# Performance work log

Hardware: AMD Instinct MI355X
Metric: run time of the kernel (lower is better)

## Reference

```python
import jax, jax.numpy as jnp
import numpy as np

DIM = 256
CDIM = 512
HEADS = 8
DIM_HEAD = 32
HID = HEADS * DIM_HEAD          # 256
MLP_DIM = int(DIM * 2.5)        # 640
B, T, TC = 8, 8192, 8192
GROUPS = 32
EPS = 1e-5


def setup_inputs() -> dict:
    key = jax.random.key(0)
    ks = jax.random.split(key, 12)
    w = lambda k, shape: jax.random.normal(k, shape, jnp.float32) * 0.02
    return {
        "x": jax.random.normal(ks[0], (B, DIM, T), jnp.float32),
        "c": jax.random.normal(ks[1], (B, CDIM, TC), jnp.float32),
        # self-attn (LinearAttention)
        "W_qkv": w(ks[2], (3 * HID, DIM)),
        "W_so": w(ks[3], (DIM, HID)), "b_so": jnp.zeros((DIM,), jnp.float32),
        "sa_g": jnp.ones((DIM,), jnp.float32), "sa_b": jnp.zeros((DIM,), jnp.float32),
        # cross-attn (LinearAttentionC)
        "W_cq": w(ks[4], (HID, DIM)),
        "W_ckv": w(ks[5], (2 * HID, CDIM)),
        "W_co": w(ks[6], (DIM, HID)), "b_co": jnp.zeros((DIM,), jnp.float32),
        "ca_g": jnp.ones((DIM,), jnp.float32), "ca_b": jnp.zeros((DIM,), jnp.float32),
        # MLP
        "W_m1": w(ks[7], (MLP_DIM, DIM)), "b_m1": jnp.zeros((MLP_DIM,), jnp.float32),
        "W_m2": w(ks[8], (DIM, MLP_DIM)), "b_m2": jnp.zeros((DIM,), jnp.float32),
        # pre-norms
        "nm_g": jnp.ones((DIM,), jnp.float32), "nm_b": jnp.zeros((DIM,), jnp.float32),
        "nm1_g": jnp.ones((DIM,), jnp.float32), "nm1_b": jnp.zeros((DIM,), jnp.float32),
        "nm2_g": jnp.ones((DIM,), jnp.float32), "nm2_b": jnp.zeros((DIM,), jnp.float32),
        "nm3_g": jnp.ones((CDIM,), jnp.float32), "nm3_b": jnp.zeros((CDIM,), jnp.float32),
    }


def group_norm(x, g, b):
    Bx, C, Tx = x.shape
    xg = x.reshape(Bx, GROUPS, C // GROUPS, Tx)
    mu = xg.mean(axis=(2, 3), keepdims=True)
    var = ((xg - mu) ** 2).mean(axis=(2, 3), keepdims=True)
    xn = ((xg - mu) * jax.lax.rsqrt(var + EPS)).reshape(Bx, C, Tx)
    return xn * g[None, :, None] + b[None, :, None]


def conv1(x, W, b=None):
    # 1x1 Conv1d == channel matmul: W [out, in], x [b, in, t]
    y = jnp.einsum('oc,bct->bot', W, x)
    return y if b is None else y + b[None, :, None]


def split_heads(t):
    Bx, HC, Tx = t.shape
    return t.reshape(Bx, HEADS, HC // HEADS, Tx)  # b h c t


def linear_attention(q, k, v):
    # q,k,v: [b, h, d, t]
    scale = DIM_HEAD ** -0.5
    q = jax.nn.softmax(q, axis=-2) * scale   # softmax over feature dim d
    k = jax.nn.softmax(k, axis=-1)           # softmax over time t
    ctx = jnp.einsum('bhdn,bhen->bhde', k, v)   # [b,h,d,e] tiny per-head context
    out = jnp.einsum('bhde,bhdn->bhen', ctx, q)
    Bx, H, E, Tx = out.shape
    return out.reshape(Bx, H * E, Tx)  # b (h c) t


def reference(x, c, W_qkv, W_so, b_so, sa_g, sa_b,
              W_cq, W_ckv, W_co, b_co, ca_g, ca_b,
              W_m1, b_m1, W_m2, b_m2,
              nm_g, nm_b, nm1_g, nm1_b, nm2_g, nm2_b, nm3_g, nm3_b):
    # --- self linear attention + residual ---
    h = group_norm(x, nm_g, nm_b)
    q, k, v = map(split_heads, jnp.split(conv1(h, W_qkv), 3, axis=1))
    o = linear_attention(q, k, v)
    o = group_norm(conv1(o, W_so, b_so), sa_g, sa_b)
    x = o + x
    # --- cross linear attention + residual ---
    h = group_norm(x, nm1_g, nm1_b)
    cn = group_norm(c, nm3_g, nm3_b)
    q = split_heads(conv1(h, W_cq))
    k, v = map(split_heads, jnp.split(conv1(cn, W_ckv), 2, axis=1))
    o = linear_attention(q, k, v)
    o = group_norm(conv1(o, W_co, b_co), ca_g, ca_b)
    x = o + x
    # --- SiLU MLP + residual ---
    h = group_norm(x, nm2_g, nm2_b)
    h = jax.nn.silu(conv1(h, W_m1, b_m1))
    x = conv1(h, W_m2, b_m2) + x
    return x
```

## Files before the change

### kernel.cpp

```cpp
#include <hip/hip_runtime.h>
#include <cmath>

typedef unsigned short u16;
typedef __attribute__((ext_vector_type(8))) __bf16 bf16x8;
typedef __attribute__((ext_vector_type(4))) float f32x4;

#define DEV static __device__ __forceinline__

DEV float b2f(u16 u){ union{unsigned i; float f;} v; v.i=((unsigned)u)<<16; return v.f; }
DEV u16 f2b(float f){ union{float f; unsigned i;} v; v.f=f; unsigned r = v.i + 0x7FFFu + ((v.i>>16)&1u); return (u16)(r>>16); }

#define GLL(g,l) __builtin_amdgcn_global_load_lds((const __attribute__((address_space(1))) void*)(g), (__attribute__((address_space(3))) void*)(l), 16, 0, 0)

__global__ void k_zero(float* p, int n){ int i = blockIdx.x*256+threadIdx.x; if(i<n) p[i]=0.f; }

__global__ void k_cvtall(const float* __restrict__ s0,const float* __restrict__ s1,
                         const float* __restrict__ s2,const float* __restrict__ s3,
                         const float* __restrict__ s4,const float* __restrict__ s5,
                         const float* __restrict__ s6, u16* __restrict__ d){
  int i = blockIdx.x*256 + threadIdx.x;
  if (i >= 983040) return;
  const float* s; int off;
  if      (i < 196608){ s=s0; off=0; }
  else if (i < 262144){ s=s1; off=196608; }
  else if (i < 327680){ s=s2; off=262144; }
  else if (i < 589824){ s=s3; off=327680; }
  else if (i < 655360){ s=s4; off=589824; }
  else if (i < 819200){ s=s5; off=655360; }
  else                { s=s6; off=819200; }
  d[i] = f2b(s[i-off]);
}

__global__ void k_stats_ct(const float* __restrict__ x, const float* __restrict__ c,
                           float* __restrict__ statx, float* __restrict__ statc){
  const bool isc = blockIdx.x >= 256;
  const int blk = isc ? blockIdx.x - 256 : blockIdx.x;
  const int n = isc ? 131072 : 65536;
  const float* src = isc ? c : x;
  float* stat = isc ? statc : statx;
  const long base = (long)blk * n;
  float s=0.f, s2=0.f;
  const float4* xp = (const float4*)(src+base);
  const int n4 = n>>2;
  for (int i=threadIdx.x; i<n4; i+=256){
    float4 v = xp[i];
    s  += v.x+v.y+v.z+v.w;
    s2 += v.x*v.x+v.y*v.y+v.z*v.z+v.w*v.w;
  }
  __shared__ float a[256], a2[256];
  a[threadIdx.x]=s; a2[threadIdx.x]=s2;
  __syncthreads();
  for (int off=128; off>0; off>>=1){
    if (threadIdx.x < off){ a[threadIdx.x]+=a[threadIdx.x+off]; a2[threadIdx.x]+=a2[threadIdx.x+off]; }
    __syncthreads();
  }
  if (threadIdx.x==0){
    const float mu = a[0]/n;
    const float var = a2[0]/n - mu*mu;
    stat[blk*2]   = mu;
    stat[blk*2+1] = rsqrtf(var + 1e-5f);
  }
}

template<bool WF32>
__global__ void k_trans(const float* __restrict__ src, float* __restrict__ dstF,
                        u16* __restrict__ dstB, const float* __restrict__ stat,
                        const float* __restrict__ gw, const float* __restrict__ bw,
                        int C, int chsh){
  const int b = blockIdx.z;
  const int t0 = blockIdx.x*64, c0 = blockIdx.y*64;
  __shared__ float tile[64][65];
  #pragma unroll
  for (int p=0;p<4;p++){
    const int cc = (threadIdx.x>>4) + p*16, tt = (threadIdx.x&15)*4;
    const float4 v = *(const float4*)&src[((long)b*C + c0+cc)*8192 + t0+tt];
    tile[cc][tt+0]=v.x; tile[cc][tt+1]=v.y; tile[cc][tt+2]=v.z; tile[cc][tt+3]=v.w;
  }
  __syncthreads();
  #pragma unroll
  for (int p=0;p<4;p++){
    const int tt = (threadIdx.x>>4) + p*16, c4 = (threadIdx.x&15)*4;
    float raw[4]; u16 nbi[4];
    #pragma unroll
    for (int j=0;j<4;j++){
      raw[j] = tile[c4+j][tt];
      const int c = c0+c4+j, gr = c>>chsh;
      const float mu = stat[(b*32+gr)*2], rs = stat[(b*32+gr)*2+1];
      nbi[j] = f2b((raw[j]-mu)*rs*gw[c]+bw[c]);
    }
    const long db = ((long)b*8192 + t0+tt)*C + c0+c4;
    ushort4 nb; nb.x=nbi[0]; nb.y=nbi[1]; nb.z=nbi[2]; nb.w=nbi[3];
    *(ushort4*)&dstB[db] = nb;
    if (WF32){ float4 rv = {raw[0],raw[1],raw[2],raw[3]}; *(float4*)&dstF[db] = rv; }
  }
}

template<bool OUTB, bool BIAS, bool SILU, bool RES, bool STATS>
__global__ __launch_bounds__(256,2) void k_gemm(
    const u16* __restrict__ A, const u16* __restrict__ W,
    float* __restrict__ outF, u16* __restrict__ outB,
    const float* __restrict__ bias, const float* __restrict__ res,
    float* __restrict__ stat, int K, int O)
{
  __shared__ u16 As[128*64];
  __shared__ u16 Ws[128*64];
  __shared__ float sb[128][2];
  const int tid = threadIdx.x;
  const int wv = tid>>6, lane = tid&63;
  const long t0 = (long)blockIdx.y*128;
  const int o0 = blockIdx.x*128;
  const int wt = (wv>>1)*64, wo = (wv&1)*64;
  const int lr = lane>>3, lc = (lane&7)*8;
  f32x4 acc[4][4] = {};
  for (int kc = 0; kc < K; kc += 64){
    #pragma unroll
    for (int it = 0; it < 4; ++it){
      const int r = wv*32 + it*8;
      GLL(A + (t0 + r + lr)*(long)K + kc + lc, &As[r*64]);
      GLL(W + (long)(o0 + r + lr)*K + kc + lc, &Ws[r*64]);
    }
    __syncthreads();
    #pragma unroll
    for (int ks=0; ks<2; ++ks){
      const int kb = ks*32 + (lane>>4)*8;
      bf16x8 af[4], bfr[4];
      #pragma unroll
      for (int i=0;i<4;i++) af[i]  = *(const bf16x8*)&As[(wt + i*16 + (lane&15))*64 + kb];
      #pragma unroll
      for (int j=0;j<4;j++) bfr[j] = *(const bf16x8*)&Ws[(wo + j*16 + (lane&15))*64 + kb];
      #pragma unroll
      for (int i=0;i<4;i++)
        #pragma unroll
        for (int j=0;j<4;j++)
          acc[i][j] = __builtin_amdgcn_mfma_f32_16x16x32_bf16(af[i], bfr[j], acc[i][j], 0, 0, 0);
    }
    __syncthreads();
  }
  if (STATS){
    if (tid < 128){ sb[tid][0]=0.f; sb[tid][1]=0.f; }
    __syncthreads();
  }
  const int q = lane>>4, cc = lane&15;
  #pragma unroll
  for (int j=0;j<4;j++){
    const int o = o0 + wo + j*16 + cc;
    const float bv = BIAS ? bias[o] : 0.f;
    float ts=0.f, ts2=0.f;
    #pragma unroll
    for (int i=0;i<4;i++){
      const long tb = t0 + wt + i*16 + q*4;
      #pragma unroll
      for (int r=0;r<4;r++){
        float v = acc[i][j][r] + bv;
        if (SILU) v = v * (1.f/(1.f + __expf(-v)));
        const long idx = (tb + r)*(long)O + o;
        if (RES) v += res[idx];
        if (STATS){ ts += v; ts2 += v*v; }
        if (OUTB) outB[idx] = f2b(v); else outF[idx] = v;
      }
    }
    if (STATS){
      const int ol = wo + j*16 + cc;
      atomicAdd(&sb[ol][0], ts);
      atomicAdd(&sb[ol][1], ts2);
    }
  }
  if (STATS){
    __syncthreads();
    if (tid < 16){
      float u=0.f, u2=0.f;
      #pragma unroll
      for (int j2=0;j2<8;j2++){ u += sb[tid*8+j2][0]; u2 += sb[tid*8+j2][1]; }
      const int bb = (int)(t0>>13);
      atomicAdd(&stat[(bb*32 + (o0>>3) + tid)*2],   u);
      atomicAdd(&stat[(bb*32 + (o0>>3) + tid)*2+1], u2);
    }
  }
}

__global__ __launch_bounds__(256,2) void k_ctx(const u16* __restrict__ kvp, float* __restrict__ part,
                      int stride, int koff, int voff){
  const int tid = threadIdx.x;
  const int b = blockIdx.x >> 6, seg = blockIdx.x & 63;
  const int h = tid>>5, d = tid&31;
  __shared__ u16 kb[16][256];
  __shared__ float vf[16][260];
  float acc[32];
  #pragma unroll
  for (int e=0;e<32;e++) acc[e]=0.f;
  float ks = 0.f;
  const long rb = ((long)b*8192 + seg*128)*stride;
  const int w = tid>>6, sub = tid&63;
  for (int tc=0; tc<128; tc+=16){
    #pragma unroll
    for (int p=0;p<4;p++){
      const int row = p*4 + w;
      const long rowbase = rb + (long)(tc+row)*stride;
      if (sub < 32){
        uint4 val = *(const uint4*)(kvp + rowbase + koff + sub*8);
        *(uint4*)&kb[row][sub*8] = val;
      } else {
        const int s2 = sub-32;
        uint4 val = *(const uint4*)(kvp + rowbase + voff + s2*8);
        const u16* vs = (const u16*)&val;
        float4 f0 = {b2f(vs[0]),b2f(vs[1]),b2f(vs[2]),b2f(vs[3])};
        float4 f1 = {b2f(vs[4]),b2f(vs[5]),b2f(vs[6]),b2f(vs[7])};
        *(float4*)&vf[row][s2*8] = f0;
        *(float4*)&vf[row][s2*8+4] = f1;
      }
    }
    __syncthreads();
    #pragma unroll
    for (int r=0;r<16;r++){
      const float kpv = __expf(b2f(kb[r][h*32+d]));
      ks += kpv;
      #pragma unroll
      for (int e4=0;e4<8;e4++){
        const float4 v4 = *(const float4*)&vf[r][h*32+e4*4];
        acc[e4*4+0] += kpv*v4.x; acc[e4*4+1] += kpv*v4.y;
        acc[e4*4+2] += kpv*v4.z; acc[e4*4+3] += kpv*v4.w;
      }
    }
    __syncthreads();
  }
  float* pb = part + (long)blockIdx.x*8448;
  #pragma unroll
  for (int e=0;e<32;e++) pb[e*256 + tid] = acc[e];
  pb[8192 + tid] = ks;
}

__global__ void k_ctxred(const float* __restrict__ part, float* __restrict__ ctx,
                         float* __restrict__ ksumF){
  if (blockIdx.x >= 256){
    const int j = (blockIdx.x-256)*256 + threadIdx.x;
    #pragma unroll
    for (int q=0;q<4;q++){
      const int idx = j*4+q;
      const int b = idx>>8, cch = idx&255;
      float s=0.f;
      for (int g=0; g<64; g++) s += part[((long)(b*64+g))*8448 + 8192 + cch];
      ksumF[idx] = s;
    }
    return;
  }
  const int i = blockIdx.x*256 + threadIdx.x;
  const int b = i>>13, r = i&8191;
  float s=0.f;
  for (int g=0; g<64; g++) s += part[((long)(b*64+g))*8448 + r];
  ctx[i] = s;
}

__global__ void k_attnout(const u16* __restrict__ q, const float* __restrict__ ctx,
                          const float* __restrict__ ksumF,
                          u16* __restrict__ out, int stride, int qoff){
  const int b = blockIdx.x >> 8, t0 = (blockIdx.x & 255)*32;
  __shared__ float cs[8512];
  for (int i=threadIdx.x; i<8192; i+=256){
    const int e=i>>8, cch=i&255;
    cs[(cch>>5)*1064 + (cch&31)*33 + e] = ctx[(b<<13) + i] / ksumF[b*256 + cch];
  }
  __syncthreads();
  const int t = t0 + (threadIdx.x>>3), h = threadIdx.x&7;
  const u16* qp = q + ((long)b*8192 + t)*stride + qoff + h*32;
  uint4 qv[4];
  #pragma unroll
  for (int j=0;j<4;j++) qv[j] = ((const uint4*)qp)[j];
  const u16* qs = (const u16*)qv;
  float qe[32]; float ssum = 0.f;
  #pragma unroll
  for (int dd=0; dd<32; dd++){ qe[dd] = __expf(b2f(qs[dd])); ssum += qe[dd]; }
  const float inv = 0.17677669529663687f / ssum;
  float o[32];
  #pragma unroll
  for (int e=0;e<32;e++) o[e]=0.f;
  const float* ch = &cs[h*1064];
  #pragma unroll
  for (int dd=0; dd<32; dd++){
    const float w = qe[dd]*inv;
    #pragma unroll
    for (int e=0;e<32;e++) o[e] += w * ch[dd*33+e];
  }
  u16 ob[32];
  #pragma unroll
  for (int e=0;e<32;e++) ob[e] = f2b(o[e]);
  uint4* op = (uint4*)(out + ((long)b*8192 + t)*256 + h*32);
  const uint4* obv = (const uint4*)ob;
  #pragma unroll
  for (int j=0;j<4;j++) op[j] = obv[j];
}

__global__ void k_gnres(const u16* __restrict__ conv, float* __restrict__ xr,
                        const float* __restrict__ sums_in, float* __restrict__ sums_out,
                        const float* __restrict__ g, const float* __restrict__ bt){
  const int blk = blockIdx.x;
  const int b = blk>>7;
  const long base = (long)blk*4096;
  const int tid = threadIdx.x;
  const int c0 = (tid<<2)&255;
  const int gr = c0>>3;
  const float s = sums_in[(b*32+gr)*2], s2 = sums_in[(b*32+gr)*2+1];
  const float mu = s*(1.f/65536.f);
  const float rs = rsqrtf(s2*(1.f/65536.f) - mu*mu + 1e-5f);
  float gg[4], bb[4];
  #pragma unroll
  for (int j=0;j<4;j++){ gg[j] = g[c0+j]*rs; bb[j] = bt[c0+j] - mu*gg[j]; }
  float ts=0.f, ts2=0.f;
  for (int it=0; it<16; ++it){
    const long i4 = base + it*256 + tid;
    ushort4 cv = ((const ushort4*)conv)[i4];
    float4 rv = ((const float4*)xr)[i4];
    float ci[4] = {b2f(cv.x),b2f(cv.y),b2f(cv.z),b2f(cv.w)};
    float ri[4] = {rv.x,rv.y,rv.z,rv.w};
    float ov[4];
    #pragma unroll
    for (int j=0;j<4;j++){
      ov[j] = ci[j]*gg[j] + bb[j] + ri[j];
      ts += ov[j]; ts2 += ov[j]*ov[j];
    }
    float4 o4 = {ov[0],ov[1],ov[2],ov[3]};
    ((float4*)xr)[i4] = o4;
  }
  __shared__ float grp[32][2];
  if (tid<32){ grp[tid][0]=0.f; grp[tid][1]=0.f; }
  __syncthreads();
  atomicAdd(&grp[gr][0], ts);
  atomicAdd(&grp[gr][1], ts2);
  __syncthreads();
  if (tid<32){
    atomicAdd(&sums_out[(b*32+tid)*2],   grp[tid][0]);
    atomicAdd(&sums_out[(b*32+tid)*2+1], grp[tid][1]);
  }
}

__global__ void k_gnapply(const float* __restrict__ x, u16* __restrict__ o,
                          const float* __restrict__ sums, const float* __restrict__ g,
                          const float* __restrict__ bt){
  const long i4 = (long)blockIdx.x*256 + threadIdx.x;
  const int b = (int)(i4 >> 19);
  const int c0 = (int)((i4<<2) & 255);
  float4 v = ((const float4*)x)[i4];
  float vi[4] = {v.x,v.y,v.z,v.w};
  u16 obi[4];
  #pragma unroll
  for (int j=0;j<4;j++){
    const int c = c0+j, gr=c>>3;
    const float s = sums[(b*32+gr)*2], s2 = sums[(b*32+gr)*2+1];
    const float mu = s*(1.f/65536.f);
    const float rs = rsqrtf(s2*(1.f/65536.f)-mu*mu+1e-5f);
    obi[j] = f2b((vi[j]-mu)*rs*g[c]+bt[c]);
  }
  ushort4 ob; ob.x=obi[0]; ob.y=obi[1]; ob.z=obi[2]; ob.w=obi[3];
  ((ushort4*)o)[i4] = ob;
}

__global__ void k_final(const float* __restrict__ y, float* __restrict__ out){
  const int b = blockIdx.z;
  const int t0 = blockIdx.x*64, c0 = blockIdx.y*64;
  __shared__ float tile[64][65];
  #pragma unroll
  for (int p=0;p<4;p++){
    const int tt = (threadIdx.x>>4) + p*16, c4 = (threadIdx.x&15)*4;
    const float4 v = *(const float4*)&y[((long)b*8192 + t0+tt)*256 + c0+c4];
    tile[c4+0][tt]=v.x; tile[c4+1][tt]=v.y; tile[c4+2][tt]=v.z; tile[c4+3][tt]=v.w;
  }
  __syncthreads();
  #pragma unroll
  for (int p=0;p<4;p++){
    const int cc = (threadIdx.x>>4) + p*16, t4 = (threadIdx.x&15)*4;
    float4 v = {tile[cc][t4], tile[cc][t4+1], tile[cc][t4+2], tile[cc][t4+3]};
    *(float4*)&out[((long)b*256 + c0+cc)*8192 + t0+t4] = v;
  }
}

extern "C" void kernel_launch(void* const* d_in, const int* in_sizes, int n_in,
                              void* d_out, int out_size, void* d_ws, size_t ws_size,
                              hipStream_t stream){
  (void)in_sizes; (void)n_in; (void)out_size; (void)ws_size;
  const float* x   = (const float*)d_in[0];
  const float* c   = (const float*)d_in[1];
  const float* W_qkv=(const float*)d_in[2];
  const float* W_so =(const float*)d_in[3];
  const float* b_so =(const float*)d_in[4];
  const float* sa_g =(const float*)d_in[5];
  const float* sa_b =(const float*)d_in[6];
  const float* W_cq =(const float*)d_in[7];
  const float* W_ckv=(const float*)d_in[8];
  const float* W_co =(const float*)d_in[9];
  const float* b_co =(const float*)d_in[10];
  const float* ca_g =(const float*)d_in[11];
  const float* ca_b =(const float*)d_in[12];
  const float* W_m1 =(const float*)d_in[13];
  const float* b_m1 =(const float*)d_in[14];
  const float* W_m2 =(const float*)d_in[15];
  const float* b_m2 =(const float*)d_in[16];
  const float* nm_g =(const float*)d_in[17];
  const float* nm_b =(const float*)d_in[18];
  const float* nm1_g=(const float*)d_in[19];
  const float* nm1_b=(const float*)d_in[20];
  const float* nm2_g=(const float*)d_in[21];
  const float* nm2_b=(const float*)d_in[22];
  const float* nm3_g=(const float*)d_in[23];
  const float* nm3_b=(const float*)d_in[24];
  float* out = (float*)d_out;

  char* ws = (char*)d_ws;
  const size_t MB = 1024ull*1024ull;
  u16* wbf  = (u16*)ws;
  u16* wQKV = wbf;
  u16* wSO  = wbf + 196608;
  u16* wCQ  = wbf + 262144;
  u16* wCKV = wbf + 327680;
  u16* wCO  = wbf + 589824;
  u16* wM1  = wbf + 655360;
  u16* wM2  = wbf + 819200;
  float* stats = (float*)(ws + 2*MB);
  float* xstat = stats;
  float* cstat = stats + 512;
  float* so_sum= stats + 1024;
  float* x1_sum= stats + 1536;
  float* co_sum= stats + 2048;
  float* x2_sum= stats + 2560;
  float* ksumF = stats + 3072;
  float* ctxb  = stats + 8192;
  float* xT    = (float*)(ws + 4*MB);
  u16*   hbf   = (u16*)(ws + 68*MB);
  float* part  = (float*)(ws + 68*MB);
  u16*   cnbf  = (u16*)(ws + 100*MB);
  u16*   qkvb  = (u16*)(ws + 164*MB);
  u16*   kvb   = (u16*)(ws + 264*MB);
  u16*   convb = (u16*)(ws + 264*MB);
  float* convF = (float*)(ws + 264*MB);
  u16*   attno = (u16*)(ws + 328*MB);

  k_zero<<<12,256,0,stream>>>(stats+1024, 3072-1024+1024);
  k_cvtall<<<3840,256,0,stream>>>(W_qkv, W_so, W_cq, W_ckv, W_co, W_m1, W_m2, wbf);

  k_stats_ct<<<512,256,0,stream>>>(x, c, xstat, cstat);
  k_trans<true ><<<dim3(128,4,8),256,0,stream>>>(x, xT, hbf, xstat, nm_g, nm_b, 256, 3);
  k_trans<false><<<dim3(128,8,8),256,0,stream>>>(c, nullptr, cnbf, cstat, nm3_g, nm3_b, 512, 4);
  k_gemm<true,false,false,false,false><<<dim3(6,512),256,0,stream>>>(hbf, wQKV, nullptr, qkvb, nullptr, nullptr, nullptr, 256, 768);
  k_ctx<<<512,256,0,stream>>>(qkvb, part, 768, 256, 512);
  k_ctxred<<<258,256,0,stream>>>(part, ctxb, ksumF);
  k_attnout<<<2048,256,0,stream>>>(qkvb, ctxb, ksumF, attno, 768, 0);
  k_gemm<true,true,false,false,true><<<dim3(2,512),256,0,stream>>>(attno, wSO, nullptr, convb, b_so, nullptr, so_sum, 256, 256);
  k_gnres<<<1024,256,0,stream>>>(convb, xT, so_sum, x1_sum, sa_g, sa_b);

  k_gnapply<<<16384,256,0,stream>>>(xT, hbf, x1_sum, nm1_g, nm1_b);
  k_gemm<true,false,false,false,false><<<dim3(2,512),256,0,stream>>>(hbf, wCQ, nullptr, qkvb, nullptr, nullptr, nullptr, 256, 256);
  k_gemm<true,false,false,false,false><<<dim3(4,512),256,0,stream>>>(cnbf, wCKV, nullptr, kvb, nullptr, nullptr, nullptr, 512, 512);
  k_ctx<<<512,256,0,stream>>>(kvb, part, 512, 0, 256);
  k_ctxred<<<258,256,0,stream>>>(part, ctxb, ksumF);
  k_attnout<<<2048,256,0,stream>>>(qkvb, ctxb, ksumF, attno, 256, 0);
  k_gemm<true,true,false,false,true><<<dim3(2,512),256,0,stream>>>(attno, wCO, nullptr, convb, b_co, nullptr, co_sum, 256, 256);
  k_gnres<<<1024,256,0,stream>>>(convb, xT, co_sum, x2_sum, ca_g, ca_b);

  k_gnapply<<<16384,256,0,stream>>>(xT, hbf, x2_sum, nm2_g, nm2_b);
  k_gemm<true,true,true,false,false><<<dim3(5,512),256,0,stream>>>(hbf, wM1, nullptr, qkvb, b_m1, nullptr, nullptr, 256, 640);
  k_gemm<false,true,false,true,false><<<dim3(2,512),256,0,stream>>>(qkvb, wM2, convF, nullptr, b_m2, xT, nullptr, 640, 256);
  k_final<<<dim3(128,4,8),256,0,stream>>>(convF, out);
}
```

Before: 1.044 ms.

## Store residual stream in bf16, split qkv outputs, parallelize group-norm stats

```diff
diff --git a/kernel.cpp b/kernel.cpp
--- a/kernel.cpp
+++ b/kernel.cpp
@@ -31,19 +31,17 @@
   d[i] = f2b(s[i-off]);
 }
 
-__global__ void k_stats_ct(const float* __restrict__ x, const float* __restrict__ c,
-                           float* __restrict__ statx, float* __restrict__ statc){
-  const bool isc = blockIdx.x >= 256;
-  const int blk = isc ? blockIdx.x - 256 : blockIdx.x;
-  const int n = isc ? 131072 : 65536;
-  const float* src = isc ? c : x;
-  float* stat = isc ? statc : statx;
-  const long base = (long)blk * n;
+__global__ void k_stats2(const float* __restrict__ x, const float* __restrict__ c,
+                         float* __restrict__ statx, float* __restrict__ statc){
+  const int blk = blockIdx.x;
+  const float* src; float* stat; long base; int chunk;
+  if (blk < 2048){ chunk = blk>>3; base = (long)chunk*65536 + (long)(blk&7)*8192; src=x; stat=statx; }
+  else { const int b2 = blk-2048; chunk = b2>>4; base = (long)chunk*131072 + (long)(b2&15)*8192; src=c; stat=statc; }
+  const float4* xp = (const float4*)(src+base);
   float s=0.f, s2=0.f;
-  const float4* xp = (const float4*)(src+base);
-  const int n4 = n>>2;
-  for (int i=threadIdx.x; i<n4; i+=256){
-    float4 v = xp[i];
+  #pragma unroll
+  for (int i=0;i<8;i++){
+    float4 v = xp[i*256 + threadIdx.x];
     s  += v.x+v.y+v.z+v.w;
     s2 += v.x*v.x+v.y*v.y+v.z*v.z+v.w*v.w;
   }
@@ -55,18 +53,16 @@
     __syncthreads();
   }
   if (threadIdx.x==0){
-    const float mu = a[0]/n;
-    const float var = a2[0]/n - mu*mu;
-    stat[blk*2]   = mu;
-    stat[blk*2+1] = rsqrtf(var + 1e-5f);
-  }
-}
-
-template<bool WF32>
-__global__ void k_trans(const float* __restrict__ src, float* __restrict__ dstF,
+    atomicAdd(&stat[chunk*2],   a[0]);
+    atomicAdd(&stat[chunk*2+1], a2[0]);
+  }
+}
+
+template<bool WRAW>
+__global__ void k_trans(const float* __restrict__ src, u16* __restrict__ dstRaw,
                         u16* __restrict__ dstB, const float* __restrict__ stat,
                         const float* __restrict__ gw, const float* __restrict__ bw,
-                        int C, int chsh){
+                        int C, int chsh, float inv_n){
   const int b = blockIdx.z;
   const int t0 = blockIdx.x*64, c0 = blockIdx.y*64;
   __shared__ float tile[64][65];
@@ -80,26 +76,29 @@
   #pragma unroll
   for (int p=0;p<4;p++){
     const int tt = (threadIdx.x>>4) + p*16, c4 = (threadIdx.x&15)*4;
-    float raw[4]; u16 nbi[4];
+    u16 nbi[4], rbi[4];
     #pragma unroll
     for (int j=0;j<4;j++){
-      raw[j] = tile[c4+j][tt];
-      const int c = c0+c4+j, gr = c>>chsh;
-      const float mu = stat[(b*32+gr)*2], rs = stat[(b*32+gr)*2+1];
-      nbi[j] = f2b((raw[j]-mu)*rs*gw[c]+bw[c]);
+      const float raw = tile[c4+j][tt];
+      const int ch = c0+c4+j, gr = ch>>chsh;
+      const float s = stat[(b*32+gr)*2], s2 = stat[(b*32+gr)*2+1];
+      const float mu = s*inv_n;
+      const float rs = rsqrtf(s2*inv_n - mu*mu + 1e-5f);
+      nbi[j] = f2b((raw-mu)*rs*gw[ch]+bw[ch]);
+      rbi[j] = f2b(raw);
     }
     const long db = ((long)b*8192 + t0+tt)*C + c0+c4;
     ushort4 nb; nb.x=nbi[0]; nb.y=nbi[1]; nb.z=nbi[2]; nb.w=nbi[3];
     *(ushort4*)&dstB[db] = nb;
-    if (WF32){ float4 rv = {raw[0],raw[1],raw[2],raw[3]}; *(float4*)&dstF[db] = rv; }
-  }
-}
-
-template<bool OUTB, bool BIAS, bool SILU, bool RES, bool STATS>
+    if (WRAW){ ushort4 rv; rv.x=rbi[0]; rv.y=rbi[1]; rv.z=rbi[2]; rv.w=rbi[3]; *(ushort4*)&dstRaw[db] = rv; }
+  }
+}
+
+template<bool OUTB, bool BIAS, bool SILU, bool RES, bool STATS, bool SPLIT>
 __global__ __launch_bounds__(256,2) void k_gemm(
     const u16* __restrict__ A, const u16* __restrict__ W,
     float* __restrict__ outF, u16* __restrict__ outB,
-    const float* __restrict__ bias, const float* __restrict__ res,
+    const float* __restrict__ bias, const u16* __restrict__ res,
     float* __restrict__ stat, int K, int O)
 {
   __shared__ u16 As[128*64];
@@ -153,8 +152,10 @@
       for (int r=0;r<4;r++){
         float v = acc[i][j][r] + bv;
         if (SILU) v = v * (1.f/(1.f + __expf(-v)));
-        const long idx = (tb + r)*(long)O + o;
-        if (RES) v += res[idx];
+        long idx;
+        if (SPLIT) idx = ((long)(o>>8)<<24) + (tb + r)*256 + (o&255);
+        else       idx = (tb + r)*(long)O + o;
+        if (RES) v += b2f(res[idx]);
         if (STATS){ ts += v; ts2 += v*v; }
         if (OUTB) outB[idx] = f2b(v); else outF[idx] = v;
       }
@@ -178,8 +179,8 @@
   }
 }
 
-__global__ __launch_bounds__(256,2) void k_ctx(const u16* __restrict__ kvp, float* __restrict__ part,
-                      int stride, int koff, int voff){
+__global__ __launch_bounds__(256,2) void k_ctx(const u16* __restrict__ kp, const u16* __restrict__ vp,
+                                               float* __restrict__ part){
   const int tid = threadIdx.x;
   const int b = blockIdx.x >> 6, seg = blockIdx.x & 63;
   const int h = tid>>5, d = tid&31;
@@ -189,19 +190,19 @@
   #pragma unroll
   for (int e=0;e<32;e++) acc[e]=0.f;
   float ks = 0.f;
-  const long rb = ((long)b*8192 + seg*128)*stride;
+  const long rb = (long)b*8192 + seg*128;
   const int w = tid>>6, sub = tid&63;
   for (int tc=0; tc<128; tc+=16){
     #pragma unroll
     for (int p=0;p<4;p++){
       const int row = p*4 + w;
-      const long rowbase = rb + (long)(tc+row)*stride;
+      const long rowbase = (rb + tc + row)*256;
       if (sub < 32){
-        uint4 val = *(const uint4*)(kvp + rowbase + koff + sub*8);
+        uint4 val = *(const uint4*)(kp + rowbase + sub*8);
         *(uint4*)&kb[row][sub*8] = val;
       } else {
         const int s2 = sub-32;
-        uint4 val = *(const uint4*)(kvp + rowbase + voff + s2*8);
+        uint4 val = *(const uint4*)(vp + rowbase + s2*8);
         const u16* vs = (const u16*)&val;
         float4 f0 = {b2f(vs[0]),b2f(vs[1]),b2f(vs[2]),b2f(vs[3])};
         float4 f1 = {b2f(vs[4]),b2f(vs[5]),b2f(vs[6]),b2f(vs[7])};
@@ -251,8 +252,7 @@
 }
 
 __global__ void k_attnout(const u16* __restrict__ q, const float* __restrict__ ctx,
-                          const float* __restrict__ ksumF,
-                          u16* __restrict__ out, int stride, int qoff){
+                          const float* __restrict__ ksumF, u16* __restrict__ out){
   const int b = blockIdx.x >> 8, t0 = (blockIdx.x & 255)*32;
   __shared__ float cs[8512];
   for (int i=threadIdx.x; i<8192; i+=256){
@@ -261,7 +261,7 @@
   }
   __syncthreads();
   const int t = t0 + (threadIdx.x>>3), h = threadIdx.x&7;
-  const u16* qp = q + ((long)b*8192 + t)*stride + qoff + h*32;
+  const u16* qp = q + ((long)b*8192 + t)*256 + h*32;
   uint4 qv[4];
   #pragma unroll
   for (int j=0;j<4;j++) qv[j] = ((const uint4*)qp)[j];
@@ -289,7 +289,7 @@
   for (int j=0;j<4;j++) op[j] = obv[j];
 }
 
-__global__ void k_gnres(const u16* __restrict__ conv, float* __restrict__ xr,
+__global__ void k_gnres(const u16* __restrict__ conv, u16* __restrict__ xr,
                         const float* __restrict__ sums_in, float* __restrict__ sums_out,
                         const float* __restrict__ g, const float* __restrict__ bt){
   const int blk = blockIdx.x;
@@ -308,17 +308,17 @@
   for (int it=0; it<16; ++it){
     const long i4 = base + it*256 + tid;
     ushort4 cv = ((const ushort4*)conv)[i4];
-    float4 rv = ((const float4*)xr)[i4];
-    float ci[4] = {b2f(cv.x),b2f(cv.y),b2f(cv.z),b2f(cv.w)};
-    float ri[4] = {rv.x,rv.y,rv.z,rv.w};
+    ushort4 rv = ((const ushort4*)xr)[i4];
     float ov[4];
+    const float ci[4] = {b2f(cv.x),b2f(cv.y),b2f(cv.z),b2f(cv.w)};
+    const float ri[4] = {b2f(rv.x),b2f(rv.y),b2f(rv.z),b2f(rv.w)};
     #pragma unroll
     for (int j=0;j<4;j++){
       ov[j] = ci[j]*gg[j] + bb[j] + ri[j];
       ts += ov[j]; ts2 += ov[j]*ov[j];
     }
-    float4 o4 = {ov[0],ov[1],ov[2],ov[3]};
-    ((float4*)xr)[i4] = o4;
+    ushort4 o4; o4.x=f2b(ov[0]); o4.y=f2b(ov[1]); o4.z=f2b(ov[2]); o4.w=f2b(ov[3]);
+    ((ushort4*)xr)[i4] = o4;
   }
   __shared__ float grp[32][2];
   if (tid<32){ grp[tid][0]=0.f; grp[tid][1]=0.f; }
@@ -332,22 +332,22 @@
   }
 }
 
-__global__ void k_gnapply(const float* __restrict__ x, u16* __restrict__ o,
+__global__ void k_gnapply(const u16* __restrict__ x, u16* __restrict__ o,
                           const float* __restrict__ sums, const float* __restrict__ g,
                           const float* __restrict__ bt){
   const long i4 = (long)blockIdx.x*256 + threadIdx.x;
   const int b = (int)(i4 >> 19);
   const int c0 = (int)((i4<<2) & 255);
-  float4 v = ((const float4*)x)[i4];
-  float vi[4] = {v.x,v.y,v.z,v.w};
+  ushort4 v = ((const ushort4*)x)[i4];
+  const float vi[4] = {b2f(v.x),b2f(v.y),b2f(v.z),b2f(v.w)};
   u16 obi[4];
   #pragma unroll
   for (int j=0;j<4;j++){
-    const int c = c0+j, gr=c>>3;
+    const int ch = c0+j, gr=ch>>3;
     const float s = sums[(b*32+gr)*2], s2 = sums[(b*32+gr)*2+1];
     const float mu = s*(1.f/65536.f);
     const float rs = rsqrtf(s2*(1.f/65536.f)-mu*mu+1e-5f);
-    obi[j] = f2b((vi[j]-mu)*rs*g[c]+bt[c]);
+    obi[j] = f2b((vi[j]-mu)*rs*g[ch]+bt[ch]);
   }
   ushort4 ob; ob.x=obi[0]; ob.y=obi[1]; ob.z=obi[2]; ob.w=obi[3];
   ((ushort4*)o)[i4] = ob;
@@ -422,7 +422,7 @@
   float* x2_sum= stats + 2560;
   float* ksumF = stats + 3072;
   float* ctxb  = stats + 8192;
-  float* xT    = (float*)(ws + 4*MB);
+  u16*   xT    = (u16*)(ws + 4*MB);
   u16*   hbf   = (u16*)(ws + 68*MB);
   float* part  = (float*)(ws + 68*MB);
   u16*   cnbf  = (u16*)(ws + 100*MB);
@@ -431,31 +431,32 @@
   u16*   convb = (u16*)(ws + 264*MB);
   float* convF = (float*)(ws + 264*MB);
   u16*   attno = (u16*)(ws + 328*MB);
-
-  k_zero<<<12,256,0,stream>>>(stats+1024, 3072-1024+1024);
+  const long SEG = 1L<<24;
+
+  k_zero<<<12,256,0,stream>>>(stats, 3072);
   k_cvtall<<<3840,256,0,stream>>>(W_qkv, W_so, W_cq, W_ckv, W_co, W_m1, W_m2, wbf);
 
-  k_stats_ct<<<512,256,0,stream>>>(x, c, xstat, cstat);
-  k_trans<true ><<<dim3(128,4,8),256,0,stream>>>(x, xT, hbf, xstat, nm_g, nm_b, 256, 3);
-  k_trans<false><<<dim3(128,8,8),256,0,stream>>>(c, nullptr, cnbf, cstat, nm3_g, nm3_b, 512, 4);
-  k_gemm<true,false,false,false,false><<<dim3(6,512),256,0,stream>>>(hbf, wQKV, nullptr, qkvb, nullptr, nullptr, nullptr, 256, 768);
-  k_ctx<<<512,256,0,stream>>>(qkvb, part, 768, 256, 512);
+  k_stats2<<<6144,256,0,stream>>>(x, c, xstat, cstat);
+  k_trans<true ><<<dim3(128,4,8),256,0,stream>>>(x, xT, hbf, xstat, nm_g, nm_b, 256, 3, 1.f/65536.f);
+  k_trans<false><<<dim3(128,8,8),256,0,stream>>>(c, nullptr, cnbf, cstat, nm3_g, nm3_b, 512, 4, 1.f/131072.f);
+  k_gemm<true,false,false,false,false,true><<<dim3(6,512),256,0,stream>>>(hbf, wQKV, nullptr, qkvb, nullptr, nullptr, nullptr, 256, 768);
+  k_ctx<<<512,256,0,stream>>>(qkvb+SEG, qkvb+2*SEG, part);
   k_ctxred<<<258,256,0,stream>>>(part, ctxb, ksumF);
-  k_attnout<<<2048,256,0,stream>>>(qkvb, ctxb, ksumF, attno, 768, 0);
-  k_gemm<true,true,false,false,true><<<dim3(2,512),256,0,stream>>>(attno, wSO, nullptr, convb, b_so, nullptr, so_sum, 256, 256);
+  k_attnout<<<2048,256,0,stream>>>(qkvb, ctxb, ksumF, attno);
+  k_gemm<true,true,false,false,true,false><<<dim3(2,512),256,0,stream>>>(attno, wSO, nullptr, convb, b_so, nullptr, so_sum, 256, 256);
   k_gnres<<<1024,256,0,stream>>>(convb, xT, so_sum, x1_sum, sa_g, sa_b);
 
   k_gnapply<<<16384,256,0,stream>>>(xT, hbf, x1_sum, nm1_g, nm1_b);
-  k_gemm<true,false,false,false,false><<<dim3(2,512),256,0,stream>>>(hbf, wCQ, nullptr, qkvb, nullptr, nullptr, nullptr, 256, 256);
-  k_gemm<true,false,false,false,false><<<dim3(4,512),256,0,stream>>>(cnbf, wCKV, nullptr, kvb, nullptr, nullptr, nullptr, 512, 512);
-  k_ctx<<<512,256,0,stream>>>(kvb, part, 512, 0, 256);
+  k_gemm<true,false,false,false,false,false><<<dim3(2,512),256,0,stream>>>(hbf, wCQ, nullptr, qkvb, nullptr, nullptr, nullptr, 256, 256);
+  k_gemm<true,false,false,false,false,true><<<dim3(4,512),256,0,stream>>>(cnbf, wCKV, nullptr, kvb, nullptr, nullptr, nullptr, 512, 512);
+  k_ctx<<<512,256,0,stream>>>(kvb, kvb+SEG, part);
   k_ctxred<<<258,256,0,stream>>>(part, ctxb, ksumF);
-  k_attnout<<<2048,256,0,stream>>>(qkvb, ctxb, ksumF, attno, 256, 0);
-  k_gemm<true,true,false,false,true><<<dim3(2,512),256,0,stream>>>(attno, wCO, nullptr, convb, b_co, nullptr, co_sum, 256, 256);
+  k_attnout<<<2048,256,0,stream>>>(qkvb, ctxb, ksumF, attno);
+  k_gemm<true,true,false,false,true,false><<<dim3(2,512),256,0,stream>>>(attno, wCO, nullptr, convb, b_co, nullptr, co_sum, 256, 256);
   k_gnres<<<1024,256,0,stream>>>(convb, xT, co_sum, x2_sum, ca_g, ca_b);
 
   k_gnapply<<<16384,256,0,stream>>>(xT, hbf, x2_sum, nm2_g, nm2_b);
-  k_gemm<true,true,true,false,false><<<dim3(5,512),256,0,stream>>>(hbf, wM1, nullptr, qkvb, b_m1, nullptr, nullptr, 256, 640);
-  k_gemm<false,true,false,true,false><<<dim3(2,512),256,0,stream>>>(qkvb, wM2, convF, nullptr, b_m2, xT, nullptr, 640, 256);
+  k_gemm<true,true,true,false,false,false><<<dim3(5,512),256,0,stream>>>(hbf, wM1, nullptr, qkvb, b_m1, nullptr, nullptr, 256, 640);
+  k_gemm<false,true,false,true,false,false><<<dim3(2,512),256,0,stream>>>(qkvb, wM2, convF, nullptr, b_m2, xT, nullptr, 640, 256);
   k_final<<<dim3(128,4,8),256,0,stream>>>(convF, out);
 }
```

Measured after the change: 977.3 us. -6.4%, faster.
